# Optimization experiments

Measured on AMD Instinct MI355X. Metric: run time of the kernel, lower is better.

The kernel has to match this reference:

```python
import jax, jax.numpy as jnp
import numpy as np
import functools

EPS_L1 = 1e-12   # torch F.normalize eps
BN_EPS = 1e-5    # torch BatchNorm eps


def _sga_dir(x, k, spatial_axis, reverse):
    """Semi-global aggregation along one spatial direction.
    x: [B,C,D,H,W] cost volume, k: [B,C,5,H,W] L1-normalized guidance weights.
    Recursion (GANet eq.4): A(p,d) = w0*C(p,d) + w1*A(p-r,d) + w2*A(p-r,d-1)
                                     + w3*A(p-r,d+1) + w4*max_d' A(p-r,d').
    Boundary pixel: A = C. d+-1 out of range treated as 0.
    """
    xm = jnp.moveaxis(x, spatial_axis, 0)   # [L, B,C,D,R]
    km = jnp.moveaxis(k, spatial_axis, 0)   # [L, B,C,5,R]
    if reverse:
        xm = xm[::-1]
        km = km[::-1]

    def step(prev, inp):
        # prev: [B,C,D,R]
        xw, kw = inp                                   # [B,C,D,R], [B,C,5,R]
        w0, w1, w2, w3, w4 = (kw[:, :, i, None, :] for i in range(5))  # [B,C,1,R]
        zero = jnp.zeros_like(prev[:, :, :1])
        prev_dm = jnp.concatenate([zero, prev[:, :, :-1]], axis=2)  # A(d-1)
        prev_dp = jnp.concatenate([prev[:, :, 1:], zero], axis=2)   # A(d+1)
        prev_mx = jnp.max(prev, axis=2, keepdims=True)              # max_d A
        out = w0 * xw + w1 * prev + w2 * prev_dm + w3 * prev_dp + w4 * prev_mx
        return out, out

    a0 = xm[0]
    _, rest = jax.lax.scan(step, a0, (xm[1:], km[1:]))
    out = jnp.concatenate([a0[None], rest], axis=0)
    if reverse:
        out = out[::-1]
    return jnp.moveaxis(out, 0, spatial_axis)


def _l1_normalize(k):
    # F.normalize(k, p=1, dim=2)
    s = jnp.sum(jnp.abs(k), axis=2, keepdims=True)
    return k / jnp.maximum(s, EPS_L1)


def _bn_eval(x, scale, bias):
    # eval-mode BatchNorm3d with running_mean=0, running_var=1
    inv = scale / jnp.sqrt(1.0 + BN_EPS)
    return x * inv[None, :, None, None, None] + bias[None, :, None, None, None]


def setup_inputs() -> dict:
    key = jax.random.key(0)
    k0, k1, k2 = jax.random.split(key, 3)
    B, C, D, H, W = 1, 32, 48, 64, 128
    x = jax.random.normal(k0, (B, C, D, H, W), dtype=jnp.float32)
    g = jax.random.normal(k1, (B, 4 * C * 5, H, W), dtype=jnp.float32)
    w_refine = jax.random.normal(k2, (C, C, 3, 3, 3), dtype=jnp.float32) * 0.05
    return {
        "x": x,
        "g": g,
        "w_refine": w_refine,
        "bn1_scale": jnp.ones((C,), jnp.float32),
        "bn1_bias": jnp.zeros((C,), jnp.float32),
        "bn2_scale": jnp.ones((C,), jnp.float32),
        "bn2_bias": jnp.zeros((C,), jnp.float32),
    }


def reference(x, g, w_refine, bn1_scale, bn1_bias, bn2_scale, bn2_bias):
    B, C, D, H, W = x.shape
    rem = x
    # split g into k1..k4, each [B,C,5,H,W], L1-normalize over the 5 weights
    kall = g.reshape(B, 4, C, 5, H, W)
    # directions: left->right, right->left (axis W=4), top->down, down->top (axis H=3)
    specs = [(4, False), (4, True), (3, False), (3, True)]
    outs = [
        _sga_dir(x, _l1_normalize(kall[:, i]), ax, rev)
        for i, (ax, rev) in enumerate(specs)
    ]
    agg = functools.reduce(jnp.maximum, outs)  # max over directions (GANet eq.5)
    # refine branch: BN -> ReLU -> Conv3d(3x3x3, no bias) -> BN
    y = jax.nn.relu(_bn_eval(agg, bn1_scale, bn1_bias))
    y = jax.lax.conv_general_dilated(
        y, w_refine, window_strides=(1, 1, 1), padding=[(1, 1)] * 3,
        dimension_numbers=("NCDHW", "OIDHW", "NCDHW"))
    y = _bn_eval(y, bn2_scale, bn2_bias)
    return jax.nn.relu(y + rem)
```

## Files before the change

kernel.cpp:

```cpp
#include <hip/hip_runtime.h>

#define C_ 32
#define D_ 48
#define H_ 64
#define W_ 128
#define HW_ 8192

using short8 = __attribute__((ext_vector_type(8))) short;
using half8  = __attribute__((ext_vector_type(8))) _Float16;
using half4  = __attribute__((ext_vector_type(4))) _Float16;
using half2v = __attribute__((ext_vector_type(2))) _Float16;
using f32x4  = __attribute__((ext_vector_type(4))) float;

__device__ __forceinline__ const unsigned short* uni_ptr(const unsigned short* p) {
    unsigned long long v = (unsigned long long)p;
    unsigned lo = __builtin_amdgcn_readfirstlane((unsigned)v);
    unsigned hi = __builtin_amdgcn_readfirstlane((unsigned)(v >> 32));
    return (const unsigned short*)(((unsigned long long)hi << 32) | lo);
}

__device__ __forceinline__ float dpp_shr1z(float v) {
    int r = __builtin_amdgcn_update_dpp(0, __builtin_bit_cast(int, v), 0x138, 0xf, 0xf, true);
    return __builtin_bit_cast(float, r);
}
__device__ __forceinline__ float dpp_shl1z(float v) {
    int r = __builtin_amdgcn_update_dpp(0, __builtin_bit_cast(int, v), 0x130, 0xf, 0xf, true);
    return __builtin_bit_cast(float, r);
}
__device__ __forceinline__ float wave_max48(float v) {
#define RMAX(ctrl)                                                                              \
    {                                                                                           \
        int t_ = __builtin_amdgcn_update_dpp(__builtin_bit_cast(int, v),                        \
                                             __builtin_bit_cast(int, v), ctrl, 0xf, 0xf, false);\
        v = fmaxf(v, __builtin_bit_cast(float, t_));                                            \
    }
    RMAX(0x111) RMAX(0x112) RMAX(0x114) RMAX(0x118) RMAX(0x142) RMAX(0x143)
#undef RMAX
    int m = __builtin_amdgcn_readlane(__builtin_bit_cast(int, v), 47);
    return __builtin_bit_cast(float, m);
}

__device__ __forceinline__ uint4 pack5(float c0, float c1, float c2, float c3, float c4) {
    float s = fabsf(c0) + fabsf(c1) + fabsf(c2) + fabsf(c3) + fabsf(c4);
    float rn = __builtin_amdgcn_rcpf(fmaxf(s, 1e-12f));
    unsigned h0 = __builtin_bit_cast(unsigned short, (_Float16)(c0 * rn));
    unsigned h1 = __builtin_bit_cast(unsigned short, (_Float16)(c1 * rn));
    unsigned h2 = __builtin_bit_cast(unsigned short, (_Float16)(c2 * rn));
    unsigned h3 = __builtin_bit_cast(unsigned short, (_Float16)(c3 * rn));
    unsigned h4 = __builtin_bit_cast(unsigned short, (_Float16)(c4 * rn));
    return uint4{h0 | (h1 << 16), h2 | (h3 << 16), h4, 0u};
}

__global__ __launch_bounds__(256) void k_front(const float* __restrict__ x,
                                               const float* __restrict__ g,
                                               const float* __restrict__ wr,
                                               _Float16* __restrict__ xtb,
                                               unsigned short* __restrict__ gq,
                                               _Float16* __restrict__ wt) {
    __shared__ float sbuf[6192];
    const int t = threadIdx.x;
    const int bid = blockIdx.x;
    if (bid < 512) {
        int b = bid >> 1;
        int h0 = (bid & 1) * 32;
        int d2 = b >> 7, c = (b >> 2) & 31, w0 = (b & 3) * 32;
        const float* gp = g + (((d2 + 2) * C_ + c) * 5) * HW_;
#pragma unroll
        for (int k = 0; k < 20; ++k) {
            int j = k * 256 + t;
            int i = j >> 10, r = j & 1023;
            int hl = r >> 5, wl = r & 31;
            sbuf[i * 1056 + hl * 33 + wl] = gp[i * HW_ + (h0 + hl) * W_ + w0 + wl];
        }
        __syncthreads();
        uint4* gqo = (uint4*)gq + ((d2 + 2) * C_ + c) * HW_;
#pragma unroll
        for (int k = 0; k < 4; ++k) {
            int j = k * 256 + t;
            int wl = j >> 5, hl = j & 31;
            int s = hl * 33 + wl;
            gqo[(w0 + wl) * 64 + h0 + hl] = pack5(sbuf[s], sbuf[1056 + s], sbuf[2112 + s],
                                                  sbuf[3168 + s], sbuf[4224 + s]);
        }
    } else if (bid < 2560) {
        const int b = bid - 512;
        const int c = b >> 6, h = b & 63;
        const float4* xb4 = (const float4*)(x + c * (D_ * HW_) + h * W_);
#pragma unroll
        for (int i = 0; i < 6; ++i) {
            int idx = i * 256 + t;
            int d = idx >> 5, wq = idx & 31;
            float4 v = xb4[d * 2048 + wq];
            sbuf[d * 129 + wq * 4 + 0] = v.x;
            sbuf[d * 129 + wq * 4 + 1] = v.y;
            sbuf[d * 129 + wq * 4 + 2] = v.z;
            sbuf[d * 129 + wq * 4 + 3] = v.w;
        }
        __syncthreads();
        half4* xo4 = (half4*)(xtb + ((c * H_ + h) * W_) * D_);
#pragma unroll
        for (int i = 0; i < 6; ++i) {
            int idx = i * 256 + t;
            int w = idx / 12, dq = idx - w * 12;
            half4 hv;
#pragma unroll
            for (int k = 0; k < 4; ++k) hv[k] = (_Float16)sbuf[(dq * 4 + k) * 129 + w];
            xo4[w * 12 + dq] = hv;
        }
    } else if (bid < 4608) {
        int e = (bid - 2560) * 256 + t;
        int dir = e >> 18;
        int c = (e >> 13) & 31;
        int pos = e & 8191;
        const float* gp = g + ((dir * C_ + c) * 5) * HW_ + pos;
        ((uint4*)gq)[e] = pack5(gp[0], gp[HW_], gp[2 * HW_], gp[3 * HW_], gp[4 * HW_]);
    } else {
        int idx = (bid - 4608) * 256 + t;
        int ci = idx & 31, co = (idx >> 5) & 31, tap = idx >> 10;
        wt[(tap * 32 + co) * 32 + ci] = (_Float16)wr[(co * 32 + ci) * 27 + tap];
    }
}

template <int T, int SS, bool REV>
__device__ __forceinline__ void scan_pass(const _Float16* __restrict__ xb,
                                          const unsigned short* __restrict__ gqb,
                                          _Float16* __restrict__ ab) {
    constexpr int PF = 8;
    _Float16 xs[PF], as[PF];
    half8 gs[PF];
    float prev;
    {
        constexpr int q0 = REV ? (T - 1) : 0;
        prev = (float)xb[q0 * SS];
        float o = prev;
        if (REV) o = fmaxf(o, (float)ab[q0 * SS]);
        ab[q0 * SS] = (_Float16)o;
    }
#pragma unroll
    for (int i = 0; i < PF; ++i) {
        int q = REV ? (T - 2 - i) : (1 + i);
        xs[i] = xb[q * SS];
        gs[i] = *(const half8*)(gqb + q * 8);
        if (REV) as[i] = ab[q * SS];
    }
    auto step = [&](int pc, int slot) {
        _Float16 xv = xs[slot];
        half8 gh = gs[slot];
        float av = REV ? (float)as[slot] : 0.f;
        int pn = pc + PF;
        if (pn < T) {
            int qn = REV ? (T - 1 - pn) : pn;
            xs[slot] = xb[qn * SS];
            gs[slot] = *(const half8*)(gqb + qn * 8);
            if (REV) as[slot] = ab[qn * SS];
        }
        float mx = wave_max48(prev);
        float dm = dpp_shr1z(prev);
        float dp = dpp_shl1z(prev);
        float a = fmaf((float)gh[0], (float)xv, 0.f);
        a = fmaf((float)gh[1], prev, a);
        a = fmaf((float)gh[2], dm, a);
        a = fmaf((float)gh[3], dp, a);
        a = fmaf((float)gh[4], mx, a);
        float o = REV ? fmaxf(a, av) : a;
        int qq = REV ? (T - 1 - pc) : pc;
        ab[qq * SS] = (_Float16)o;
        prev = a;
    };
    int p = 1;
#pragma unroll 1
    for (; p + PF <= T; p += PF) {
#pragma unroll
        for (int i = 0; i < PF; ++i) step(p + i, i);
    }
#pragma unroll
    for (int i = 0; i < PF; ++i)
        if (p + i < T) step(p + i, i);
}

__global__ __launch_bounds__(256) void k_scan(const _Float16* __restrict__ xtb,
                                              const unsigned short* __restrict__ gq,
                                              _Float16* __restrict__ agg1,
                                              _Float16* __restrict__ agg2) {
    const int lane = threadIdx.x & 63;
    const int wid = threadIdx.x >> 6;
    if (lane >= 48) return;
    if (blockIdx.x < 512) {
        const int L = blockIdx.x * 4 + wid;
        const int c = L >> 6, h = L & 63;
        const int base = ((c * H_ + h) * W_) * D_ + lane;
        const _Float16* xb = xtb + base;
        _Float16* ab = agg1 + base;
        const unsigned short* g0 = uni_ptr(gq + (unsigned)((0 * C_ + c) * HW_ + h * W_) * 8);
        const unsigned short* g1 = uni_ptr(gq + (unsigned)((1 * C_ + c) * HW_ + h * W_) * 8);
        scan_pass<W_, D_, false>(xb, g0, ab);
        __builtin_amdgcn_s_waitcnt(0);
        scan_pass<W_, D_, true>(xb, g1, ab);
    } else {
        const int L = (blockIdx.x - 512) * 4 + wid;
        const int c = L >> 7, w = L & 127;
        const int base = (c * HW_ + w) * D_ + lane;
        const _Float16* xb = xtb + base;
        _Float16* ab = agg2 + base;
        const unsigned short* g2 = uni_ptr(gq + (unsigned)((2 * C_ + c) * HW_ + w * H_) * 8);
        const unsigned short* g3 = uni_ptr(gq + (unsigned)((3 * C_ + c) * HW_ + w * H_) * 8);
        scan_pass<H_, W_ * D_, false>(xb, g2, ab);
        __builtin_amdgcn_s_waitcnt(0);
        scan_pass<H_, W_ * D_, true>(xb, g3, ab);
    }
}

__global__ __launch_bounds__(256) void k_prep(const _Float16* __restrict__ agg1,
                                              const _Float16* __restrict__ agg2,
                                              const float* __restrict__ bn1s,
                                              const float* __restrict__ bn1b,
                                              _Float16* __restrict__ y2p) {
    const int t = threadIdx.x;
    if (blockIdx.x >= 1024) {
        int i = (blockIdx.x - 1024) * 256 + t;
        if (i < 143136) {
            unsigned u4i;
            if (i < 52000) {
                int slab = i / 26000, off = i % 26000;
                u4i = slab * 65 * 26000 + off;
            } else if (i < 118560) {
                int j = i - 52000;
                int h = j / 1040 + 1, r = j % 1040;
                int d = (r < 520) ? 0 : 49, off = (r < 520) ? r : r - 520;
                u4i = h * 26000 + d * 520 + off;
            } else {
                int j = i - 118560;
                int h = j / 384 + 1, r = j % 384;
                int d = (r >> 3) + 1, r2 = r & 7;
                int w = (r2 >> 2) ? 129 : 0;
                u4i = h * 26000 + d * 520 + w * 4 + (r2 & 3);
            }
            ((uint4*)y2p)[u4i] = uint4{0u, 0u, 0u, 0u};
        }
        return;
    }
    __shared__ float L[48 * 267 + 8];
    __shared__ float s_inv[32], s_b[32];
    if (t < 32) {
        s_inv[t] = bn1s[t] * rsqrtf(1.f + 1e-5f);
        s_b[t] = bn1b[t];
    }
    __syncthreads();
    const int h = blockIdx.x >> 4;
    const int w0 = (blockIdx.x & 15) * 8;
    const half4* a14 = (const half4*)agg1;
    const half4* a24 = (const half4*)agg2;
#pragma unroll
    for (int it = 0; it < 12; ++it) {
        int i = it * 256 + t;
        int c = i / 96, r = i - c * 96;
        int wi = r / 12, dq = r - wi * 12;
        int ao = ((c * H_ + h) * W_ + (w0 + wi)) * 12 + dq;
        half4 u1 = a14[ao];
        half4 u2 = a24[ao];
        float si = s_inv[c], sb = s_b[c];
#pragma unroll
        for (int k = 0; k < 4; ++k) {
            float v = fmaxf((float)u1[k], (float)u2[k]);
            L[(dq * 4 + k) * 267 + wi * 33 + c] = fmaxf(v * si + sb, 0.f);
        }
    }
    __syncthreads();
    half2v* yb2 = (half2v*)y2p;
#pragma unroll
    for (int it = 0; it < 24; ++it) {
        int j = it * 256 + t;
        int c2 = j & 15, x2 = j >> 4;
        int wi = x2 & 7, d = x2 >> 3;
        const float* lp = &L[d * 267 + wi * 33 + c2 * 2];
        half2v hv;
        hv[0] = (_Float16)lp[0];
        hv[1] = (_Float16)lp[1];
        yb2[(((h + 1) * 50 + (d + 1)) * 130 + (w0 + wi + 1)) * 16 + c2] = hv;
    }
}

__global__ __launch_bounds__(256, 3) void k_conv(const _Float16* __restrict__ y2p,
                                                 const _Float16* __restrict__ wt,
                                                 const float* __restrict__ x,
                                                 const float* __restrict__ bn2s,
                                                 const float* __restrict__ bn2b,
                                                 float* __restrict__ out) {
    __shared__ __align__(16) unsigned short ls[24576];
    const int t = threadIdx.x;
    const int lane = t & 63, wid = t >> 6;
    const int h = blockIdx.x >> 5;
    const int ow = ((blockIdx.x >> 2) & 7) * 16;
    const int od = (blockIdx.x & 3) * 12;
    {
        const int j0 = wid * 12;
#pragma unroll
        for (int jj = 0; jj < 12; ++jj) {
            int j = j0 + jj;
            int i = j * 64 + lane;
            int seg = i / 72, off = i - seg * 72;
            int kh = seg / 14, dz = seg - kh * 14;
            const _Float16* gp = y2p + (unsigned)(((h + kh) * 50 + od + dz) * 520 + ow * 4 + off) * 8;
            if (i < 3024)
                __builtin_amdgcn_global_load_lds(
                    (const __attribute__((address_space(1))) void*)gp,
                    (__attribute__((address_space(3))) void*)(ls + (unsigned)j * 512), 16, 0, 0);
        }
    }
    __syncthreads();
    const int n = lane & 15, kg = lane >> 4;
    const int dd0 = wid * 3;
    f32x4 acc[3][2] = {};
#pragma unroll
    for (int kh = 0; kh < 3; ++kh)
#pragma unroll
        for (int kd = 0; kd < 3; ++kd)
#pragma unroll
            for (int kw = 0; kw < 3; ++kw) {
                int tap = (kd * 3 + kh) * 3 + kw;
                half8 A0 = *(const half8*)(wt + (tap * 32 + n) * 32 + kg * 8);
                half8 A1 = *(const half8*)(wt + (tap * 32 + 16 + n) * 32 + kg * 8);
                const unsigned short* bp =
                    ls + (kh * 14 + dd0 + kd) * 576 + (n + kw) * 32 + kg * 8;
#pragma unroll
                for (int dd = 0; dd < 3; ++dd) {
                    half8 b = __builtin_bit_cast(half8, *(const short8*)(bp + dd * 576));
                    acc[dd][0] = __builtin_amdgcn_mfma_f32_16x16x32_f16(A0, b, acc[dd][0], 0, 0, 0);
                    acc[dd][1] = __builtin_amdgcn_mfma_f32_16x16x32_f16(A1, b, acc[dd][1], 0, 0, 0);
                }
            }
    const float rs = rsqrtf(1.f + 1e-5f);
#pragma unroll
    for (int ct = 0; ct < 2; ++ct)
#pragma unroll
        for (int r = 0; r < 4; ++r) {
            int co = ct * 16 + kg * 4 + r;
            float sc = bn2s[co] * rs, bi = bn2b[co];
#pragma unroll
            for (int dd = 0; dd < 3; ++dd) {
                int d = od + dd0 + dd;
                int addr = ((co * D_ + d) * H_ + h) * W_ + ow + n;
                float val = acc[dd][ct][r] * sc + bi;
                out[addr] = fmaxf(val + x[addr], 0.f);
            }
        }
}

extern "C" void kernel_launch(void* const* d_in, const int* in_sizes, int n_in,
                              void* d_out, int out_size, void* d_ws, size_t ws_size,
                              hipStream_t stream) {
    const float* x = (const float*)d_in[0];
    const float* g = (const float*)d_in[1];
    const float* wr = (const float*)d_in[2];
    const float* bn1s = (const float*)d_in[3];
    const float* bn1b = (const float*)d_in[4];
    const float* bn2s = (const float*)d_in[5];
    const float* bn2b = (const float*)d_in[6];
    float* out = (float*)d_out;
    char* ws = (char*)d_ws;

    _Float16* xtb = (_Float16*)ws;
    _Float16* y2p = (_Float16*)ws;
    _Float16* agg1 = (_Float16*)(ws + 33554432);
    _Float16* agg2 = (_Float16*)(ws + 58720256);
    unsigned short* gq = (unsigned short*)(ws + 83886080);
    _Float16* wt = (_Float16*)(ws + 100663296);

    k_front<<<4716, 256, 0, stream>>>(x, g, wr, xtb, gq, wt);
    k_scan<<<1536, 256, 0, stream>>>(xtb, gq, agg1, agg2);
    k_prep<<<1584, 256, 0, stream>>>(agg1, agg2, bn1s, bn1b, y2p);
    k_conv<<<2048, 256, 0, stream>>>(y2p, wt, x, bn2s, bn2b, out);
}
```

Before: 269.6 us.

## Split W-direction forward and reverse scans into separate waves with own buffers

The left-to-right and right-to-left scans along W are now run by separate blocks instead of one wave doing both in sequence. Each writes to its own aggregation buffer, and the prep kernel takes the max of three buffers instead of two. This halves the serial dependency chain for the W scans and raises the number of independent waves. The cost is an extra fp16 buffer write and read, and the new path only runs when the workspace is large enough.

```diff
diff --git a/kernel.cpp b/kernel.cpp
--- a/kernel.cpp
+++ b/kernel.cpp
@@ -121,7 +121,7 @@
     }
 }
 
-template <int T, int SS, bool REV>
+template <int T, int SS, bool REV, bool COMB>
 __device__ __forceinline__ void scan_pass(const _Float16* __restrict__ xb,
                                           const unsigned short* __restrict__ gqb,
                                           _Float16* __restrict__ ab) {
@@ -133,7 +133,7 @@
         constexpr int q0 = REV ? (T - 1) : 0;
         prev = (float)xb[q0 * SS];
         float o = prev;
-        if (REV) o = fmaxf(o, (float)ab[q0 * SS]);
+        if (COMB) o = fmaxf(o, (float)ab[q0 * SS]);
         ab[q0 * SS] = (_Float16)o;
     }
 #pragma unroll
@@ -141,18 +141,18 @@
         int q = REV ? (T - 2 - i) : (1 + i);
         xs[i] = xb[q * SS];
         gs[i] = *(const half8*)(gqb + q * 8);
-        if (REV) as[i] = ab[q * SS];
+        if (COMB) as[i] = ab[q * SS];
     }
     auto step = [&](int pc, int slot) {
         _Float16 xv = xs[slot];
         half8 gh = gs[slot];
-        float av = REV ? (float)as[slot] : 0.f;
+        float av = COMB ? (float)as[slot] : 0.f;
         int pn = pc + PF;
         if (pn < T) {
             int qn = REV ? (T - 1 - pn) : pn;
             xs[slot] = xb[qn * SS];
             gs[slot] = *(const half8*)(gqb + qn * 8);
-            if (REV) as[slot] = ab[qn * SS];
+            if (COMB) as[slot] = ab[qn * SS];
         }
         float mx = wave_max48(prev);
         float dm = dpp_shr1z(prev);
@@ -162,7 +162,7 @@
         a = fmaf((float)gh[2], dm, a);
         a = fmaf((float)gh[3], dp, a);
         a = fmaf((float)gh[4], mx, a);
-        float o = REV ? fmaxf(a, av) : a;
+        float o = COMB ? fmaxf(a, av) : a;
         int qq = REV ? (T - 1 - pc) : pc;
         ab[qq * SS] = (_Float16)o;
         prev = a;
@@ -193,9 +193,9 @@
         _Float16* ab = agg1 + base;
         const unsigned short* g0 = uni_ptr(gq + (unsigned)((0 * C_ + c) * HW_ + h * W_) * 8);
         const unsigned short* g1 = uni_ptr(gq + (unsigned)((1 * C_ + c) * HW_ + h * W_) * 8);
-        scan_pass<W_, D_, false>(xb, g0, ab);
+        scan_pass<W_, D_, false, false>(xb, g0, ab);
         __builtin_amdgcn_s_waitcnt(0);
-        scan_pass<W_, D_, true>(xb, g1, ab);
+        scan_pass<W_, D_, true, true>(xb, g1, ab);
     } else {
         const int L = (blockIdx.x - 512) * 4 + wid;
         const int c = L >> 7, w = L & 127;
@@ -204,17 +204,55 @@
         _Float16* ab = agg2 + base;
         const unsigned short* g2 = uni_ptr(gq + (unsigned)((2 * C_ + c) * HW_ + w * H_) * 8);
         const unsigned short* g3 = uni_ptr(gq + (unsigned)((3 * C_ + c) * HW_ + w * H_) * 8);
-        scan_pass<H_, W_ * D_, false>(xb, g2, ab);
+        scan_pass<H_, W_ * D_, false, false>(xb, g2, ab);
         __builtin_amdgcn_s_waitcnt(0);
-        scan_pass<H_, W_ * D_, true>(xb, g3, ab);
-    }
-}
-
-__global__ __launch_bounds__(256) void k_prep(const _Float16* __restrict__ agg1,
-                                              const _Float16* __restrict__ agg2,
-                                              const float* __restrict__ bn1s,
-                                              const float* __restrict__ bn1b,
-                                              _Float16* __restrict__ y2p) {
+        scan_pass<H_, W_ * D_, true, true>(xb, g3, ab);
+    }
+}
+
+__global__ __launch_bounds__(256) void k_scan_b(const _Float16* __restrict__ xtb,
+                                                const unsigned short* __restrict__ gq,
+                                                _Float16* __restrict__ agg1f,
+                                                _Float16* __restrict__ agg1r,
+                                                _Float16* __restrict__ agg2) {
+    const int lane = threadIdx.x & 63;
+    const int wid = threadIdx.x >> 6;
+    if (lane >= 48) return;
+    if (blockIdx.x < 1024) {
+        const int pair = blockIdx.x >> 1;
+        const int rev = blockIdx.x & 1;
+        const int L = pair * 4 + wid;
+        const int c = L >> 6, h = L & 63;
+        const int base = ((c * H_ + h) * W_) * D_ + lane;
+        const _Float16* xb = xtb + base;
+        if (!rev) {
+            const unsigned short* g0 = uni_ptr(gq + (unsigned)((0 * C_ + c) * HW_ + h * W_) * 8);
+            scan_pass<W_, D_, false, false>(xb, g0, agg1f + base);
+        } else {
+            const unsigned short* g1 = uni_ptr(gq + (unsigned)((1 * C_ + c) * HW_ + h * W_) * 8);
+            scan_pass<W_, D_, true, false>(xb, g1, agg1r + base);
+        }
+    } else {
+        const int L = (blockIdx.x - 1024) * 4 + wid;
+        const int c = L >> 7, w = L & 127;
+        const int base = (c * HW_ + w) * D_ + lane;
+        const _Float16* xb = xtb + base;
+        _Float16* ab = agg2 + base;
+        const unsigned short* g2 = uni_ptr(gq + (unsigned)((2 * C_ + c) * HW_ + w * H_) * 8);
+        const unsigned short* g3 = uni_ptr(gq + (unsigned)((3 * C_ + c) * HW_ + w * H_) * 8);
+        scan_pass<H_, W_ * D_, false, false>(xb, g2, ab);
+        __builtin_amdgcn_s_waitcnt(0);
+        scan_pass<H_, W_ * D_, true, true>(xb, g3, ab);
+    }
+}
+
+template <int NA>
+__device__ __forceinline__ void prep_body(const _Float16* __restrict__ a1,
+                                          const _Float16* __restrict__ a1r,
+                                          const _Float16* __restrict__ a2,
+                                          const float* __restrict__ bn1s,
+                                          const float* __restrict__ bn1b,
+                                          _Float16* __restrict__ y2p) {
     const int t = threadIdx.x;
     if (blockIdx.x >= 1024) {
         int i = (blockIdx.x - 1024) * 256 + t;
@@ -248,8 +286,9 @@
     __syncthreads();
     const int h = blockIdx.x >> 4;
     const int w0 = (blockIdx.x & 15) * 8;
-    const half4* a14 = (const half4*)agg1;
-    const half4* a24 = (const half4*)agg2;
+    const half4* a14 = (const half4*)a1;
+    const half4* a1r4 = (const half4*)a1r;
+    const half4* a24 = (const half4*)a2;
 #pragma unroll
     for (int it = 0; it < 12; ++it) {
         int i = it * 256 + t;
@@ -258,10 +297,14 @@
         int ao = ((c * H_ + h) * W_ + (w0 + wi)) * 12 + dq;
         half4 u1 = a14[ao];
         half4 u2 = a24[ao];
+        half4 u1r{};
+        if (NA == 3) u1r = a1r4[ao];
         float si = s_inv[c], sb = s_b[c];
 #pragma unroll
         for (int k = 0; k < 4; ++k) {
-            float v = fmaxf((float)u1[k], (float)u2[k]);
+            float v1 = (float)u1[k];
+            if (NA == 3) v1 = fmaxf(v1, (float)u1r[k]);
+            float v = fmaxf(v1, (float)u2[k]);
             L[(dq * 4 + k) * 267 + wi * 33 + c] = fmaxf(v * si + sb, 0.f);
         }
     }
@@ -278,6 +321,23 @@
         hv[1] = (_Float16)lp[1];
         yb2[(((h + 1) * 50 + (d + 1)) * 130 + (w0 + wi + 1)) * 16 + c2] = hv;
     }
+}
+
+__global__ __launch_bounds__(256) void k_prep(const _Float16* __restrict__ agg1,
+                                              const _Float16* __restrict__ agg2,
+                                              const float* __restrict__ bn1s,
+                                              const float* __restrict__ bn1b,
+                                              _Float16* __restrict__ y2p) {
+    prep_body<2>(agg1, agg1, agg2, bn1s, bn1b, y2p);
+}
+
+__global__ __launch_bounds__(256) void k_prep3(const _Float16* __restrict__ agg1f,
+                                               const _Float16* __restrict__ agg1r,
+                                               const _Float16* __restrict__ agg2,
+                                               const float* __restrict__ bn1s,
+                                               const float* __restrict__ bn1b,
+                                               _Float16* __restrict__ y2p) {
+    prep_body<3>(agg1f, agg1r, agg2, bn1s, bn1b, y2p);
 }
 
 __global__ __launch_bounds__(256, 3) void k_conv(const _Float16* __restrict__ y2p,
@@ -359,15 +419,30 @@
     float* out = (float*)d_out;
     char* ws = (char*)d_ws;
 
-    _Float16* xtb = (_Float16*)ws;
-    _Float16* y2p = (_Float16*)ws;
-    _Float16* agg1 = (_Float16*)(ws + 33554432);
-    _Float16* agg2 = (_Float16*)(ws + 58720256);
-    unsigned short* gq = (unsigned short*)(ws + 83886080);
-    _Float16* wt = (_Float16*)(ws + 100663296);
-
-    k_front<<<4716, 256, 0, stream>>>(x, g, wr, xtb, gq, wt);
-    k_scan<<<1536, 256, 0, stream>>>(xtb, gq, agg1, agg2);
-    k_prep<<<1584, 256, 0, stream>>>(agg1, agg2, bn1s, bn1b, y2p);
-    k_conv<<<2048, 256, 0, stream>>>(y2p, wt, x, bn2s, bn2b, out);
-}
+    if (ws_size >= 125884416ull) {
+        _Float16* xtb = (_Float16*)ws;
+        _Float16* y2p = (_Float16*)ws;
+        _Float16* agg1f = (_Float16*)(ws + 33554432);
+        _Float16* agg1r = (_Float16*)(ws + 58720256);
+        _Float16* agg2 = (_Float16*)(ws + 83886080);
+        unsigned short* gq = (unsigned short*)(ws + 109051904);
+        _Float16* wt = (_Float16*)(ws + 125829120);
+
+        k_front<<<4716, 256, 0, stream>>>(x, g, wr, xtb, gq, wt);
+        k_scan_b<<<2048, 256, 0, stream>>>(xtb, gq, agg1f, agg1r, agg2);
+        k_prep3<<<1584, 256, 0, stream>>>(agg1f, agg1r, agg2, bn1s, bn1b, y2p);
+        k_conv<<<2048, 256, 0, stream>>>(y2p, wt, x, bn2s, bn2b, out);
+    } else {
+        _Float16* xtb = (_Float16*)ws;
+        _Float16* y2p = (_Float16*)ws;
+        _Float16* agg1 = (_Float16*)(ws + 33554432);
+        _Float16* agg2 = (_Float16*)(ws + 58720256);
+        unsigned short* gq = (unsigned short*)(ws + 83886080);
+        _Float16* wt = (_Float16*)(ws + 100663296);
+
+        k_front<<<4716, 256, 0, stream>>>(x, g, wr, xtb, gq, wt);
+        k_scan<<<1536, 256, 0, stream>>>(xtb, gq, agg1, agg2);
+        k_prep<<<1584, 256, 0, stream>>>(agg1, agg2, bn1s, bn1b, y2p);
+        k_conv<<<2048, 256, 0, stream>>>(y2p, wt, x, bn2s, bn2b, out);
+    }
+}
```

After: 274.3 us. Within noise of the previous version (+1.7%).
